# Kernel optimization log

Hardware: AMD Instinct MI355X
Metric: run time of the kernel (lower is better)

Reference implementation:

```python
import jax, jax.numpy as jnp
import numpy as np

B, T, V, E, H, DE = 64, 52, 10000, 512, 512, 2048


def _lstm_cell(x, h, c, w_ih, w_hh, b_ih, b_hh):
    # torch.nn.LSTMCell gate order: i, f, g, o
    gates = x @ w_ih.T + h @ w_hh.T + b_ih + b_hh
    i, f, g, o = jnp.split(gates, 4, axis=-1)
    c2 = jax.nn.sigmoid(f) * c + jax.nn.sigmoid(i) * jnp.tanh(g)
    h2 = jax.nn.sigmoid(o) * jnp.tanh(c2)
    return h2, c2


def _run_dir(emb_seq, img, lens, p1, p2, fc_w, fc_b):
    # emb_seq: [B, Td, E]; img: [B, H]; lens: [B] sorted descending.
    # The torch loop slices h[:batch_size_t]; since lens is sorted descending,
    # that is equivalent to masking updates where t >= (len-1). Rows that fall
    # out of the active prefix are never read again, and their predictions stay 0.
    Bd, Td = emb_seq.shape[0], emb_seq.shape[1]
    Hd = img.shape[1]
    mask = jnp.arange(Td)[None, :] < (lens - 1)[:, None]  # [B, Td]
    z = jnp.zeros((Bd, Hd), emb_seq.dtype)

    def step(carry, xs):
        h, c, h1, c1 = carry
        x, m = xs
        m2 = m[:, None]
        hn, cn = _lstm_cell(x, h, c, *p1)
        h1n, c1n = _lstm_cell(jnp.concatenate([hn, img], axis=1), h1, c1, *p2)
        carry = (jnp.where(m2, hn, h), jnp.where(m2, cn, c),
                 jnp.where(m2, h1n, h1), jnp.where(m2, c1n, c1))
        preds = jnp.where(m2, h1n @ fc_w.T + fc_b, 0.0)  # [B, V]
        return carry, preds

    _, preds = jax.lax.scan(step, (z, z, z, z), (emb_seq.transpose(1, 0, 2), mask.T))
    return preds.transpose(1, 0, 2)  # [B, Td, V]


def setup_inputs():
    key = jax.random.key(0)
    ks = iter(jax.random.split(key, 48))

    def u(shape, a=-0.1, b=0.1):
        return jax.random.uniform(next(ks), shape, minval=a, maxval=b, dtype=jnp.float32)

    inp = {}
    inp['encoder_out'] = jax.random.normal(next(ks), (B, DE), dtype=jnp.float32)
    inp['encoded_captions'] = jax.random.randint(next(ks), (B, T), 0, V)
    cl = jax.random.randint(next(ks), (B, 1), 2, T + 1)
    inp['caption_lengths'] = cl.at[0, 0].set(T)  # ensure max decode length = T-1
    # embeddings (uniform -0.1..0.1 per init_weights)
    inp['emb_w'] = u((V, E))
    inp['emb_r_w'] = u((V, E))
    # LSTM cells: torch default init uniform(-1/sqrt(H), 1/sqrt(H))
    kH = 1.0 / np.sqrt(H)
    for name, din in [('1', E), ('2', 2 * H), ('r1', E), ('r2', 2 * H)]:
        inp['w_ih' + name] = u((4 * H, din), -kH, kH)
        inp['w_hh' + name] = u((4 * H, H), -kH, kH)
        inp['b_ih' + name] = u((4 * H,), -kH, kH)
        inp['b_hh' + name] = u((4 * H,), -kH, kH)
    kD = 1.0 / np.sqrt(DE)
    inp['img_f_w'] = u((H, DE), -kD, kD)
    inp['img_f_b'] = u((H,), -kD, kD)
    inp['img_b_w'] = u((H, DE), -kD, kD)
    inp['img_b_b'] = u((H,), -kD, kD)
    inp['fc_w'] = u((V, H))
    inp['fc_b'] = jnp.zeros((V,), jnp.float32)
    inp['fcr_w'] = u((V, H))
    inp['fcr_b'] = jnp.zeros((V,), jnp.float32)
    return inp


def reference(encoder_out, encoded_captions, caption_lengths, emb_w, emb_r_w,
              w_ih1, w_hh1, b_ih1, b_hh1, w_ih2, w_hh2, b_ih2, b_hh2,
              w_ihr1, w_hhr1, b_ihr1, b_hhr1, w_ihr2, w_hhr2, b_ihr2, b_hhr2,
              img_f_w, img_f_b, img_b_w, img_b_b, fc_w, fc_b, fcr_w, fcr_b):
    lens = caption_lengths[:, 0]
    order = jnp.argsort(-lens)  # descending, stable (jax argsort is stable)
    lens = lens[order]
    enc = encoder_out[order]
    caps = encoded_captions[order]
    Tc = caps.shape[1]
    # per-row reversal of the first len tokens; rest zero (matches torch loop)
    j = jnp.arange(Tc)[None, :]
    valid = j < lens[:, None]
    rev_idx = jnp.where(valid, lens[:, None] - 1 - j, 0)
    caps_rev = jnp.where(valid, jnp.take_along_axis(caps, rev_idx, axis=1), 0)
    emb = emb_w[caps]          # [B, T, E]
    emb_r = emb_r_w[caps_rev]  # [B, T, E]
    img_f = enc @ img_f_w.T + img_f_b
    img_r = enc @ img_b_w.T + img_b_b
    Td = Tc - 1  # max(decode_lengths); setup guarantees max(lens) == T
    preds = _run_dir(emb[:, :Td], img_f, lens,
                     (w_ih1, w_hh1, b_ih1, b_hh1), (w_ih2, w_hh2, b_ih2, b_hh2), fc_w, fc_b)
    preds_r = _run_dir(emb_r[:, :Td], img_r, lens,
                       (w_ihr1, w_hhr1, b_ihr1, b_hhr1), (w_ihr2, w_hhr2, b_ihr2, b_hhr2), fcr_w, fcr_b)
    return preds, preds_r, caps, caps_rev, lens - 1, order
```

## Files before the change

kernel.cpp:

```cpp
#include <hip/hip_runtime.h>
#include <stdint.h>

#define B64   64
#define T52   52
#define TD    51
#define V10K  10000
#define MP    3328
#define MR    3264
#define NPFC  10112

typedef float  f32x4  __attribute__((ext_vector_type(4)));
typedef __bf16 bf16x8 __attribute__((ext_vector_type(8)));
typedef unsigned int u32x4 __attribute__((ext_vector_type(4)));
typedef unsigned short ushort_t;

__device__ inline unsigned short f2bf(float f) {
  unsigned u = __builtin_bit_cast(unsigned, f);
  u += 0x7fffu + ((u >> 16) & 1u);
  return (unsigned short)(u >> 16);
}
__device__ inline unsigned pack2(float a, float b) {
  return (unsigned)f2bf(a) | ((unsigned)f2bf(b) << 16);
}
__device__ inline float sigm(float x) { return 1.f / (1.f + expf(-x)); }

__device__ inline void store2_sc(ushort_t* p, unsigned v) {
  asm volatile("global_store_short %0, %1, off sc1" :: "v"(p), "v"(v) : "memory");
}
__device__ inline void loadA16(const ushort_t* a, u32x4 (&h)[16]) {
  asm volatile(
    "global_load_dwordx4 %0,  %16, off sc1\n\t"
    "global_load_dwordx4 %1,  %16, off offset:64 sc1\n\t"
    "global_load_dwordx4 %2,  %16, off offset:128 sc1\n\t"
    "global_load_dwordx4 %3,  %16, off offset:192 sc1\n\t"
    "global_load_dwordx4 %4,  %16, off offset:256 sc1\n\t"
    "global_load_dwordx4 %5,  %16, off offset:320 sc1\n\t"
    "global_load_dwordx4 %6,  %16, off offset:384 sc1\n\t"
    "global_load_dwordx4 %7,  %16, off offset:448 sc1\n\t"
    "global_load_dwordx4 %8,  %16, off offset:512 sc1\n\t"
    "global_load_dwordx4 %9,  %16, off offset:576 sc1\n\t"
    "global_load_dwordx4 %10, %16, off offset:640 sc1\n\t"
    "global_load_dwordx4 %11, %16, off offset:704 sc1\n\t"
    "global_load_dwordx4 %12, %16, off offset:768 sc1\n\t"
    "global_load_dwordx4 %13, %16, off offset:832 sc1\n\t"
    "global_load_dwordx4 %14, %16, off offset:896 sc1\n\t"
    "global_load_dwordx4 %15, %16, off offset:960 sc1\n\t"
    "s_waitcnt vmcnt(0)"
    : "=&v"(h[0]),"=&v"(h[1]),"=&v"(h[2]),"=&v"(h[3]),
      "=&v"(h[4]),"=&v"(h[5]),"=&v"(h[6]),"=&v"(h[7]),
      "=&v"(h[8]),"=&v"(h[9]),"=&v"(h[10]),"=&v"(h[11]),
      "=&v"(h[12]),"=&v"(h[13]),"=&v"(h[14]),"=&v"(h[15])
    : "v"(a) : "memory");
}
__device__ inline void loadA32(const ushort_t* a, const ushort_t* b,
                               u32x4 (&ha)[16], u32x4 (&hb)[16]) {
  asm volatile(
    "global_load_dwordx4 %0,  %32, off sc1\n\t"
    "global_load_dwordx4 %1,  %32, off offset:64 sc1\n\t"
    "global_load_dwordx4 %2,  %32, off offset:128 sc1\n\t"
    "global_load_dwordx4 %3,  %32, off offset:192 sc1\n\t"
    "global_load_dwordx4 %4,  %32, off offset:256 sc1\n\t"
    "global_load_dwordx4 %5,  %32, off offset:320 sc1\n\t"
    "global_load_dwordx4 %6,  %32, off offset:384 sc1\n\t"
    "global_load_dwordx4 %7,  %32, off offset:448 sc1\n\t"
    "global_load_dwordx4 %8,  %32, off offset:512 sc1\n\t"
    "global_load_dwordx4 %9,  %32, off offset:576 sc1\n\t"
    "global_load_dwordx4 %10, %32, off offset:640 sc1\n\t"
    "global_load_dwordx4 %11, %32, off offset:704 sc1\n\t"
    "global_load_dwordx4 %12, %32, off offset:768 sc1\n\t"
    "global_load_dwordx4 %13, %32, off offset:832 sc1\n\t"
    "global_load_dwordx4 %14, %32, off offset:896 sc1\n\t"
    "global_load_dwordx4 %15, %32, off offset:960 sc1\n\t"
    "global_load_dwordx4 %16, %33, off sc1\n\t"
    "global_load_dwordx4 %17, %33, off offset:64 sc1\n\t"
    "global_load_dwordx4 %18, %33, off offset:128 sc1\n\t"
    "global_load_dwordx4 %19, %33, off offset:192 sc1\n\t"
    "global_load_dwordx4 %20, %33, off offset:256 sc1\n\t"
    "global_load_dwordx4 %21, %33, off offset:320 sc1\n\t"
    "global_load_dwordx4 %22, %33, off offset:384 sc1\n\t"
    "global_load_dwordx4 %23, %33, off offset:448 sc1\n\t"
    "global_load_dwordx4 %24, %33, off offset:512 sc1\n\t"
    "global_load_dwordx4 %25, %33, off offset:576 sc1\n\t"
    "global_load_dwordx4 %26, %33, off offset:640 sc1\n\t"
    "global_load_dwordx4 %27, %33, off offset:704 sc1\n\t"
    "global_load_dwordx4 %28, %33, off offset:768 sc1\n\t"
    "global_load_dwordx4 %29, %33, off offset:832 sc1\n\t"
    "global_load_dwordx4 %30, %33, off offset:896 sc1\n\t"
    "global_load_dwordx4 %31, %33, off offset:960 sc1\n\t"
    "s_waitcnt vmcnt(0)"
    : "=&v"(ha[0]),"=&v"(ha[1]),"=&v"(ha[2]),"=&v"(ha[3]),
      "=&v"(ha[4]),"=&v"(ha[5]),"=&v"(ha[6]),"=&v"(ha[7]),
      "=&v"(ha[8]),"=&v"(ha[9]),"=&v"(ha[10]),"=&v"(ha[11]),
      "=&v"(ha[12]),"=&v"(ha[13]),"=&v"(ha[14]),"=&v"(ha[15]),
      "=&v"(hb[0]),"=&v"(hb[1]),"=&v"(hb[2]),"=&v"(hb[3]),
      "=&v"(hb[4]),"=&v"(hb[5]),"=&v"(hb[6]),"=&v"(hb[7]),
      "=&v"(hb[8]),"=&v"(hb[9]),"=&v"(hb[10]),"=&v"(hb[11]),
      "=&v"(hb[12]),"=&v"(hb[13]),"=&v"(hb[14]),"=&v"(hb[15])
    : "v"(a), "v"(b) : "memory");
}

__global__ void k_prep(const int* __restrict__ cl, const int* __restrict__ caps,
                       float* __restrict__ out_caps, float* __restrict__ out_capr,
                       float* __restrict__ out_lm1, float* __restrict__ out_ord,
                       int* __restrict__ order_i, int* __restrict__ lensm1_i,
                       int* __restrict__ nvtab, int* __restrict__ capsS,
                       int* __restrict__ capsRev, int* __restrict__ cumtab,
                       int* __restrict__ rowmap)
{
  __shared__ int L[64], O[64], Ls_s[64], Cum[65];
  __shared__ int C_s[64][T52];
  int i = threadIdx.x;
  L[i] = cl[i];
  __syncthreads();
  if (i == 0) {
    for (int a = 0; a < 64; ++a) O[a] = a;
    for (int a = 1; a < 64; ++a) {
      int key = O[a], kl = L[key], b = a - 1;
      while (b >= 0 && L[O[b]] < kl) { O[b + 1] = O[b]; --b; }
      O[b + 1] = key;
    }
  }
  __syncthreads();
  int src = O[i];
  int Ls  = L[src];
  Ls_s[i] = Ls;
  order_i[i]  = src;
  lensm1_i[i] = Ls - 1;
  out_lm1[i]  = (float)(Ls - 1);
  out_ord[i]  = (float)src;
  for (int t = 0; t < T52; ++t) {
    int c = caps[src * T52 + t];
    C_s[i][t] = c;
    capsS[i * T52 + t]    = c;
    out_caps[i * T52 + t] = (float)c;
  }
  __syncthreads();
  for (int j = 0; j < T52; ++j) {
    int rv = (j < Ls) ? C_s[i][Ls - 1 - j] : 0;
    capsRev[i * T52 + j]  = rv;
    out_capr[i * T52 + j] = (float)rv;
  }
  if (i == 0) {
    int s = 0;
    for (int b = 0; b < 64; ++b) { Cum[b] = s; s += Ls_s[b] - 1; }
    Cum[64] = s;
  }
  __syncthreads();
  cumtab[i] = Cum[i];
  if (i == 0) cumtab[64] = Cum[64];
  for (int t = 0; t < Ls - 1; ++t) rowmap[Cum[i] + t] = i * TD + t;
  {
    int Mc = Cum[64];
    int invBase = Mc + i * TD - Cum[i];
    for (int t = Ls - 1; t < TD; ++t)
      rowmap[invBase + (t - (Ls - 1))] = i * TD + t;
  }
  if (i < TD) {
    int nv = 0;
    for (int r = 0; r < 64; ++r) nv += (Ls_s[r] - 1 > i) ? 1 : 0;
    nvtab[i] = nv;
  }
}

__global__ void k_convert(const float* __restrict__ w_ih1, const float* __restrict__ w_ihr1,
                          const float* __restrict__ fc_w, const float* __restrict__ fcr_w,
                          const float* __restrict__ b_ih1, const float* __restrict__ b_hh1,
                          const float* __restrict__ b_ihr1, const float* __restrict__ b_hhr1,
                          const float* __restrict__ w_hh1, const float* __restrict__ w_hhr1,
                          const float* __restrict__ w_ih2, const float* __restrict__ w_ihr2,
                          const float* __restrict__ w_hh2, const float* __restrict__ w_hhr2,
                          const float* __restrict__ img_f_w, const float* __restrict__ img_b_w,
                          const float* __restrict__ b_ih2, const float* __restrict__ b_hh2,
                          const float* __restrict__ b_ihr2, const float* __restrict__ b_hhr2,
                          const float* __restrict__ enc, const int* __restrict__ order_i,
                          const float* __restrict__ emb_w, const float* __restrict__ emb_r_w,
                          const int* __restrict__ capsS, const int* __restrict__ capsRev,
                          const int* __restrict__ rowmap, const int* __restrict__ cumtab,
                          ushort_t* __restrict__ wih1bf, ushort_t* __restrict__ fcwbf,
                          ushort_t* __restrict__ whh1bf, ushort_t* __restrict__ wih2Lbf,
                          ushort_t* __restrict__ whh2bf, ushort_t* __restrict__ wih2Ibf,
                          ushort_t* __restrict__ imgwbf, ushort_t* __restrict__ encbf,
                          ushort_t* __restrict__ embA,
                          float* __restrict__ biasg1, float* __restrict__ biasg2)
{
  long long gid = (long long)blockIdx.x * blockDim.x + threadIdx.x;
  const long long C1 = 2048LL * 512 / 8;
  const long long CF = (long long)NPFC * 512 / 8;
  const long long CPD = (long long)MP * 512 / 8;
  const long long bs  = 2 * C1 + 2 * CF;
  const long long bs2 = bs + 6 * C1;
  const long long bs3 = bs2 + 2 * C1;
  const long long bs4 = bs3 + 2 * C1;
  const long long bs5 = bs4 + 32768;
  const long long bs6 = bs5 + 2 * CPD;
  if (gid < 2 * C1) {
    int dir = gid >= C1; long long cid = gid - (long long)dir * C1;
    const float* s = (dir ? w_ihr1 : w_ih1) + cid * 8;
    ushort_t* d = wih1bf + (long long)dir * 2048 * 512 + cid * 8;
    uint4 v;
    v.x = pack2(s[0], s[1]); v.y = pack2(s[2], s[3]);
    v.z = pack2(s[4], s[5]); v.w = pack2(s[6], s[7]);
    *(uint4*)d = v;
  } else if (gid < bs) {
    long long g2 = gid - 2 * C1; int dir = g2 >= CF;
    long long cid = g2 - (long long)dir * CF;
    long long row = cid >> 6; int k8 = (int)(cid & 63) * 8;
    ushort_t* d = fcwbf + (long long)dir * NPFC * 512 + row * 512 + k8;
    uint4 v;
    if (row < V10K) {
      const float* s = (dir ? fcr_w : fc_w) + row * 512 + k8;
      v.x = pack2(s[0], s[1]); v.y = pack2(s[2], s[3]);
      v.z = pack2(s[4], s[5]); v.w = pack2(s[6], s[7]);
    } else { v.x = v.y = v.z = v.w = 0u; }
    *(uint4*)d = v;
  } else if (gid < bs2) {
    long long e = gid - bs;
    int arr = (int)(e / (2 * C1));
    long long d2 = e - (long long)arr * 2 * C1;
    int dir = d2 >= C1;
    long long cid = d2 - (long long)dir * C1;
    long long row = cid >> 6; int k8 = (int)(cid & 63) * 8;
    const float* s;
    ushort_t* d;
    if (arr == 0)      { s = (dir ? w_hhr1 : w_hh1) + row * 512  + k8; d = whh1bf; }
    else if (arr == 1) { s = (dir ? w_ihr2 : w_ih2) + row * 1024 + k8; d = wih2Lbf; }
    else               { s = (dir ? w_hhr2 : w_hh2) + row * 512  + k8; d = whh2bf; }
    d += (long long)dir * 2048 * 512 + cid * 8;
    uint4 v;
    v.x = pack2(s[0], s[1]); v.y = pack2(s[2], s[3]);
    v.z = pack2(s[4], s[5]); v.w = pack2(s[6], s[7]);
    *(uint4*)d = v;
  } else if (gid < bs3) {
    long long e = gid - bs2; int dir = e >= C1;
    long long cid = e - (long long)dir * C1;
    long long row = cid >> 6; int k8 = (int)(cid & 63) * 8;
    const float* s = (dir ? w_ihr2 : w_ih2) + row * 1024 + 512 + k8;
    ushort_t* d = wih2Ibf + (long long)dir * 2048 * 512 + cid * 8;
    uint4 v;
    v.x = pack2(s[0], s[1]); v.y = pack2(s[2], s[3]);
    v.z = pack2(s[4], s[5]); v.w = pack2(s[6], s[7]);
    *(uint4*)d = v;
  } else if (gid < bs4) {
    long long e = gid - bs3; int dir = e >= C1;
    long long cid = e - (long long)dir * C1;
    long long row = cid >> 8; int c8 = (int)(cid & 255) * 8;
    const float* s = (dir ? img_b_w : img_f_w) + row * 2048 + c8;
    ushort_t* d = imgwbf + (long long)dir * 512 * 2048 + cid * 8;
    uint4 v;
    v.x = pack2(s[0], s[1]); v.y = pack2(s[2], s[3]);
    v.z = pack2(s[4], s[5]); v.w = pack2(s[6], s[7]);
    *(uint4*)d = v;
  } else if (gid < bs5) {
    long long cid = gid - bs4;
    int m = (int)(cid >> 8); int c8 = (int)(cid & 255) * 8;
    const float* s = enc + (long long)order_i[m & 63] * 2048 + c8;
    ushort_t* d = encbf + cid * 8;
    uint4 v;
    v.x = pack2(s[0], s[1]); v.y = pack2(s[2], s[3]);
    v.z = pack2(s[4], s[5]); v.w = pack2(s[6], s[7]);
    *(uint4*)d = v;
  } else if (gid < bs6) {
    long long e = gid - bs5;
    int dir = e >= CPD; long long cid = e - (long long)dir * CPD;
    int c = (int)(cid >> 6); int k8 = (int)(cid & 63) * 8;
    ushort_t* d = embA + (long long)dir * MP * 512 + (long long)c * 512 + k8;
    uint4 v;
    if (c < cumtab[64]) {
      int m = rowmap[c];
      int b = m / TD, t = m - b * TD;
      int row = dir ? capsRev[b * T52 + t] : capsS[b * T52 + t];
      const float* s = (dir ? emb_r_w : emb_w) + (long long)row * 512 + k8;
      v.x = pack2(s[0], s[1]); v.y = pack2(s[2], s[3]);
      v.z = pack2(s[4], s[5]); v.w = pack2(s[6], s[7]);
    } else { v.x = v.y = v.z = v.w = 0u; }
    *(uint4*)d = v;
  } else {
    long long g3 = gid - bs6;
    if (g3 < 4096) {
      int dir = g3 >= 2048; int j = (int)(g3 & 2047);
      biasg1[dir * 2048 + j] = dir ? (b_ihr1[j] + b_hhr1[j]) : (b_ih1[j] + b_hh1[j]);
    } else if (g3 < 8192) {
      long long g4 = g3 - 4096;
      int dir = g4 >= 2048; int j = (int)(g4 & 2047);
      biasg2[dir * 2048 + j] = dir ? (b_ihr2[j] + b_hhr2[j]) : (b_ih2[j] + b_hh2[j]);
    }
  }
}

template<int MODE>
__global__ __launch_bounds__(256)
void k_gemm(const ushort_t* __restrict__ A0, long long As,
            const ushort_t* __restrict__ B0, long long Bs,
            const float* __restrict__ bias0, const float* __restrict__ bias1,
            void* __restrict__ out0, long long Os,
            int Nreal, int K, const int* __restrict__ mlim)
{
  long long tm = (long long)blockIdx.x * 128;
  if (mlim && tm >= mlim[64]) return;
  __shared__ ushort_t Ab[128 * 32];
  __shared__ ushort_t Bb[128 * 32];
  int dirz = blockIdx.z;
  const ushort_t* A = A0 + dirz * As;
  const ushort_t* Bm = B0 + dirz * Bs;
  const float* bias = dirz ? bias1 : bias0;
  int tid = threadIdx.x;
  int lane = tid & 63, wid = tid >> 6;
  int wr = wid >> 1, wc = wid & 1;
  long long tn = (long long)blockIdx.y * 128;
  f32x4 acc[4][4] = {};
  int c0 = tid, c1 = tid + 256;
  const ushort_t* Ag0 = A + (tm + (c0 >> 2)) * K + (c0 & 3) * 8;
  const ushort_t* Ag1 = A + (tm + (c1 >> 2)) * K + (c1 & 3) * 8;
  const ushort_t* Bg0 = Bm + (tn + (c0 >> 2)) * K + (c0 & 3) * 8;
  const ushort_t* Bg1 = Bm + (tn + (c1 >> 2)) * K + (c1 & 3) * 8;
  int KK = K >> 5;
  for (int kk = 0; kk < KK; ++kk) {
    uint4 va0 = *(const uint4*)(Ag0 + kk * 32);
    uint4 va1 = *(const uint4*)(Ag1 + kk * 32);
    uint4 vb0 = *(const uint4*)(Bg0 + kk * 32);
    uint4 vb1 = *(const uint4*)(Bg1 + kk * 32);
    __syncthreads();
    *(uint4*)&Ab[c0 * 8] = va0;
    *(uint4*)&Ab[c1 * 8] = va1;
    *(uint4*)&Bb[c0 * 8] = vb0;
    *(uint4*)&Bb[c1 * 8] = vb1;
    __syncthreads();
    int koff = (lane >> 4) * 8;
    bf16x8 av[4], bv[4];
    #pragma unroll
    for (int mi = 0; mi < 4; ++mi)
      av[mi] = *(const bf16x8*)&Ab[(wr * 64 + mi * 16 + (lane & 15)) * 32 + koff];
    #pragma unroll
    for (int ni = 0; ni < 4; ++ni)
      bv[ni] = *(const bf16x8*)&Bb[(wc * 64 + ni * 16 + (lane & 15)) * 32 + koff];
    #pragma unroll
    for (int mi = 0; mi < 4; ++mi)
      #pragma unroll
      for (int ni = 0; ni < 4; ++ni)
        acc[mi][ni] = __builtin_amdgcn_mfma_f32_16x16x32_bf16(av[mi], bv[ni], acc[mi][ni], 0, 0, 0);
  }
  #pragma unroll
  for (int mi = 0; mi < 4; ++mi) {
    #pragma unroll
    for (int rr = 0; rr < 4; ++rr) {
      long long m = tm + wr * 64 + mi * 16 + ((lane >> 4) * 4) + rr;
      if (MODE == 0) {
        float* orow = (float*)out0 + dirz * Os + m * (long long)Nreal;
        #pragma unroll
        for (int ni = 0; ni < 4; ++ni) {
          int n = (int)tn + wc * 64 + ni * 16 + (lane & 15);
          orow[n] = acc[mi][ni][rr] + bias[n];
        }
      } else if (MODE == 2) {
        float bm = bias[m];
        float* orow = (float*)out0 + dirz * Os + m * (long long)Nreal;
        #pragma unroll
        for (int ni = 0; ni < 4; ++ni) {
          int n = (int)tn + wc * 64 + ni * 16 + (lane & 15);
          if (n < Nreal) orow[n] = acc[mi][ni][rr] + bm;
        }
      } else {
        ushort_t* orow = (ushort_t*)out0 + dirz * Os + m * (long long)Nreal;
        #pragma unroll
        for (int ni = 0; ni < 4; ++ni) {
          int n = (int)tn + wc * 64 + ni * 16 + (lane & 15);
          orow[n] = f2bf(acc[mi][ni][rr] + bias[n]);
        }
      }
    }
  }
}

__global__ __launch_bounds__(256)
void k_fc(const ushort_t* __restrict__ A0, const ushort_t* __restrict__ B0,
          const float* __restrict__ bias0, const float* __restrict__ bias1,
          float* __restrict__ out0, const int* __restrict__ rowmap,
          const int* __restrict__ cumtab)
{
  const long long PRED = (long long)MR * V10K;
  int Mc = cumtab[64];
  int bid = blockIdx.x;
  int xcd = bid & 7, slot = bid >> 3;
  int q = slot / 26, mi = slot % 26;
  int G = xcd + 8 * q;
  if (G >= 158) return;
  int dirz = G & 1, ni = G >> 1;
  long long tm = (long long)mi * 128;
  long long tn = (long long)ni * 128;
  float* out = out0 + (long long)dirz * PRED;
  int tid = threadIdx.x;
  if (tm >= Mc) {
    int row = tid >> 1, hf = tid & 1;
    long long c = tm + row;
    if (c < MR) {
      int m = rowmap[c];
      float* orow = out + (long long)m * V10K;
      float4 z = {0.f, 0.f, 0.f, 0.f};
      int col0 = (int)tn + hf * 64;
      #pragma unroll
      for (int qq = 0; qq < 16; ++qq) {
        int col = col0 + qq * 4;
        if (col < V10K) *(float4*)(orow + col) = z;
      }
    }
    return;
  }
  __shared__ ushort_t Ab[128 * 32];
  __shared__ ushort_t Bb[128 * 32];
  const ushort_t* A = A0 + (long long)dirz * MP * 512;
  const ushort_t* Bm = B0 + (long long)dirz * NPFC * 512;
  const float* bias = dirz ? bias1 : bias0;
  int lane = tid & 63, wid = tid >> 6;
  int wr = wid >> 1, wc = wid & 1;
  f32x4 acc[4][4] = {};
  int c0 = tid, c1 = tid + 256;
  const ushort_t* Ag0 = A + (tm + (c0 >> 2)) * 512 + (c0 & 3) * 8;
  const ushort_t* Ag1 = A + (tm + (c1 >> 2)) * 512 + (c1 & 3) * 8;
  const ushort_t* Bg0 = Bm + (tn + (c0 >> 2)) * 512 + (c0 & 3) * 8;
  const ushort_t* Bg1 = Bm + (tn + (c1 >> 2)) * 512 + (c1 & 3) * 8;
  for (int kk = 0; kk < 16; ++kk) {
    uint4 va0 = *(const uint4*)(Ag0 + kk * 32);
    uint4 va1 = *(const uint4*)(Ag1 + kk * 32);
    uint4 vb0 = *(const uint4*)(Bg0 + kk * 32);
    uint4 vb1 = *(const uint4*)(Bg1 + kk * 32);
    __syncthreads();
    *(uint4*)&Ab[c0 * 8] = va0;
    *(uint4*)&Ab[c1 * 8] = va1;
    *(uint4*)&Bb[c0 * 8] = vb0;
    *(uint4*)&Bb[c1 * 8] = vb1;
    __syncthreads();
    int koff = (lane >> 4) * 8;
    bf16x8 av[4], bv[4];
    #pragma unroll
    for (int mi2 = 0; mi2 < 4; ++mi2)
      av[mi2] = *(const bf16x8*)&Ab[(wr * 64 + mi2 * 16 + (lane & 15)) * 32 + koff];
    #pragma unroll
    for (int ni2 = 0; ni2 < 4; ++ni2)
      bv[ni2] = *(const bf16x8*)&Bb[(wc * 64 + ni2 * 16 + (lane & 15)) * 32 + koff];
    #pragma unroll
    for (int mi2 = 0; mi2 < 4; ++mi2)
      #pragma unroll
      for (int ni2 = 0; ni2 < 4; ++ni2)
        acc[mi2][ni2] = __builtin_amdgcn_mfma_f32_16x16x32_bf16(av[mi2], bv[ni2], acc[mi2][ni2], 0, 0, 0);
  }
  #pragma unroll
  for (int mi2 = 0; mi2 < 4; ++mi2) {
    #pragma unroll
    for (int rr = 0; rr < 4; ++rr) {
      long long c = tm + wr * 64 + mi2 * 16 + ((lane >> 4) * 4) + rr;
      if (c < MR) {
        int m = rowmap[c];
        bool val = (c < Mc);
        float* orow = out + (long long)m * V10K;
        #pragma unroll
        for (int ni2 = 0; ni2 < 4; ++ni2) {
          int n = (int)tn + wc * 64 + ni2 * 16 + (lane & 15);
          if (n < V10K) orow[n] = val ? (acc[mi2][ni2][rr] + bias[n]) : 0.f;
        }
      }
    }
  }
}

__global__ __launch_bounds__(128, 1)
void k_rec(const ushort_t* __restrict__ whh1bf, const ushort_t* __restrict__ wih2Lbf,
           const ushort_t* __restrict__ whh2bf, const float* __restrict__ xg1,
           const float* __restrict__ xg2imgT,
           ushort_t* __restrict__ h1hist,
           ushort_t* __restrict__ h2buf,
           ushort_t* __restrict__ h2allbf,
           const int* __restrict__ nvtab, const int* __restrict__ cumtab,
           int* __restrict__ slots)
{
  const int bid = blockIdx.x;
  const bool isL2 = bid >= 128;
  const int idx = isL2 ? bid - 128 : bid;
  const int dir = idx >> 6, sub = idx & 63, half = sub >> 5, ht = sub & 31;
  const int tid = threadIdx.x;
  const int lane = tid & 63, mt = tid >> 6;
  const int l15 = lane & 15, l4 = lane >> 4;
  const int jl = ht * 16 + l15;
  const int rbase = half * 32 + mt * 16;
  const int r0 = rbase + l4 * 4;

  __shared__ ushort_t Wl[32768];
  __shared__ ushort_t Wi[32768];
  __shared__ int nv_s[64];
  __shared__ int cum_s[64];

  {
    const ushort_t* src = (isL2 ? whh2bf : whh1bf) + (long long)dir * 2048 * 512;
    #pragma unroll
    for (int i = 0; i < 32; ++i) {
      int c = tid + i * 128;
      int nl = c >> 6;
      int kb = (c & 63) * 16;
      int row = (nl >> 4) * 512 + ht * 16 + (nl & 15);
      u32x4 v = *(const u32x4*)(src + (long long)row * 512 + (long long)(c & 63) * 8);
      *(u32x4*)((char*)Wl + nl * 1024 + (kb ^ ((nl & 7) << 4))) = v;
    }
    if (isL2) {
      const ushort_t* src2 = wih2Lbf + (long long)dir * 2048 * 512;
      #pragma unroll
      for (int i = 0; i < 32; ++i) {
        int c = tid + i * 128;
        int nl = c >> 6;
        int kb = (c & 63) * 16;
        int row = (nl >> 4) * 512 + ht * 16 + (nl & 15);
        u32x4 v = *(const u32x4*)(src2 + (long long)row * 512 + (long long)(c & 63) * 8);
        *(u32x4*)((char*)Wi + nl * 1024 + (kb ^ ((nl & 7) << 4))) = v;
      }
    }
    if (tid < TD) nv_s[tid] = nvtab[tid];
    if (tid < 64) cum_s[tid] = cumtab[tid];
  }
  __syncthreads();

  int* aS = slots + (dir * 2 + half) * 32;
  int* bS = slots + 128 + (dir * 2 + half) * 32;

  if (!isL2) {
    f32x4 creg = {0.f, 0.f, 0.f, 0.f};
    for (int t = 0; t < TD; ++t) {
      bool act = (rbase < nv_s[t]);
      float xs[4][4];
      if (act) {
        const float* xb = xg1 + (long long)dir * MP * 2048;
        #pragma unroll
        for (int rr = 0; rr < 4; ++rr) {
          const float* xr = xb + (long long)(cum_s[r0 + rr] + t) * 2048;
          #pragma unroll
          for (int g = 0; g < 4; ++g)
            xs[g][rr] = xr[g * 512 + jl];
        }
      }
      if (t > 0) {
        if (mt == 0) {
          for (;;) {
            int v = __hip_atomic_load(&aS[lane & 31], __ATOMIC_RELAXED, __HIP_MEMORY_SCOPE_AGENT);
            if (__all(v >= t)) break;
          }
        }
        __syncthreads();
      }
      if (act) {
        const ushort_t* hsrc = h1hist + ((long long)t * 2 + dir) * (64 * 512);
        u32x4 hv[16];
        loadA16(hsrc + (long long)(rbase + l15) * 512 + l4 * 8, hv);
        f32x4 acc[4] = {};
        #pragma unroll
        for (int kk = 0; kk < 16; ++kk) {
          bf16x8 av = __builtin_bit_cast(bf16x8, hv[kk]);
          int kb = kk * 64 + l4 * 16;
          #pragma unroll
          for (int g = 0; g < 4; ++g) {
            bf16x8 bv = *(const bf16x8*)((const char*)Wl + (g * 16 + l15) * 1024 + (kb ^ ((l15 & 7) << 4)));
            acc[g] = __builtin_amdgcn_mfma_f32_16x16x32_bf16(av, bv, acc[g], 0, 0, 0);
          }
        }
        ushort_t* hdst = h1hist + ((long long)(t + 1) * 2 + dir) * (64 * 512);
        f32x4 cn;
        #pragma unroll
        for (int rr = 0; rr < 4; ++rr) {
          float gi = acc[0][rr] + xs[0][rr];
          float gf = acc[1][rr] + xs[1][rr];
          float gg = acc[2][rr] + xs[2][rr];
          float go = acc[3][rr] + xs[3][rr];
          float c = sigm(gf) * creg[rr] + sigm(gi) * tanhf(gg);
          float h = sigm(go) * tanhf(c);
          cn[rr] = c;
          store2_sc(hdst + (long long)(r0 + rr) * 512 + jl, (unsigned)f2bf(h));
        }
        creg = cn;
      }
      __syncthreads();
      if (tid == 0)
        __hip_atomic_store(&aS[ht], t + 1, __ATOMIC_RELAXED, __HIP_MEMORY_SCOPE_AGENT);
    }
  } else {
    f32x4 xv2[4];
    {
      const float* xg = xg2imgT + (long long)dir * (2048 * 64);
      #pragma unroll
      for (int g = 0; g < 4; ++g)
        xv2[g] = *(const f32x4*)(xg + (long long)(g * 512 + jl) * 64 + r0);
    }
    f32x4 creg = {0.f, 0.f, 0.f, 0.f};
    for (int t = 0; t < TD; ++t) {
      if (mt == 0) {
        for (;;) {
          int va = __hip_atomic_load(&aS[lane & 31], __ATOMIC_RELAXED, __HIP_MEMORY_SCOPE_AGENT);
          int vb = __hip_atomic_load(&bS[lane & 31], __ATOMIC_RELAXED, __HIP_MEMORY_SCOPE_AGENT);
          if (__all((va >= t + 1) & (vb >= t))) break;
        }
      }
      __syncthreads();
      int nv = nv_s[t];
      if (rbase < nv) {
        const ushort_t* h1s = h1hist + ((long long)(t + 1) * 2 + dir) * (64 * 512);
        const ushort_t* h2s = h2buf + ((long long)((t + 1) & 1) * 2 + dir) * (64 * 512);
        u32x4 ha[16], hb[16];
        loadA32(h1s + (long long)(rbase + l15) * 512 + l4 * 8,
                h2s + (long long)(rbase + l15) * 512 + l4 * 8, ha, hb);
        f32x4 acc[4] = {};
        #pragma unroll
        for (int kk = 0; kk < 16; ++kk) {
          bf16x8 av = __builtin_bit_cast(bf16x8, ha[kk]);
          int kb = kk * 64 + l4 * 16;
          #pragma unroll
          for (int g = 0; g < 4; ++g) {
            bf16x8 bv = *(const bf16x8*)((const char*)Wi + (g * 16 + l15) * 1024 + (kb ^ ((l15 & 7) << 4)));
            acc[g] = __builtin_amdgcn_mfma_f32_16x16x32_bf16(av, bv, acc[g], 0, 0, 0);
          }
        }
        #pragma unroll
        for (int kk = 0; kk < 16; ++kk) {
          bf16x8 av = __builtin_bit_cast(bf16x8, hb[kk]);
          int kb = kk * 64 + l4 * 16;
          #pragma unroll
          for (int g = 0; g < 4; ++g) {
            bf16x8 bv = *(const bf16x8*)((const char*)Wl + (g * 16 + l15) * 1024 + (kb ^ ((l15 & 7) << 4)));
            acc[g] = __builtin_amdgcn_mfma_f32_16x16x32_bf16(av, bv, acc[g], 0, 0, 0);
          }
        }
        ushort_t* h2n = h2buf + ((long long)(t & 1) * 2 + dir) * (64 * 512);
        ushort_t* h2a = h2allbf + (long long)dir * MP * 512;
        f32x4 cn;
        #pragma unroll
        for (int rr = 0; rr < 4; ++rr) {
          float gi = acc[0][rr] + xv2[0][rr];
          float gf = acc[1][rr] + xv2[1][rr];
          float gg = acc[2][rr] + xv2[2][rr];
          float go = acc[3][rr] + xv2[3][rr];
          float c = sigm(gf) * creg[rr] + sigm(gi) * tanhf(gg);
          float h = sigm(go) * tanhf(c);
          cn[rr] = c;
          ushort_t hbb = f2bf(h);
          store2_sc(h2n + (long long)(r0 + rr) * 512 + jl, (unsigned)hbb);
          if (r0 + rr < nv)
            h2a[((long long)(cum_s[r0 + rr] + t)) * 512 + jl] = hbb;
        }
        creg = cn;
      }
      __syncthreads();
      if (tid == 0)
        __hip_atomic_store(&bS[ht], t + 1, __ATOMIC_RELAXED, __HIP_MEMORY_SCOPE_AGENT);
    }
  }
}

extern "C" void kernel_launch(void* const* d_in, const int* in_sizes, int n_in,
                              void* d_out, int out_size, void* d_ws, size_t ws_size,
                              hipStream_t stream)
{
  const float* enc     = (const float*)d_in[0];
  const int*   caps    = (const int*)d_in[1];
  const int*   cl      = (const int*)d_in[2];
  const float* emb_w   = (const float*)d_in[3];
  const float* emb_r_w = (const float*)d_in[4];
  const float* w_ih1   = (const float*)d_in[5];
  const float* w_hh1   = (const float*)d_in[6];
  const float* b_ih1   = (const float*)d_in[7];
  const float* b_hh1   = (const float*)d_in[8];
  const float* w_ih2   = (const float*)d_in[9];
  const float* w_hh2   = (const float*)d_in[10];
  const float* b_ih2   = (const float*)d_in[11];
  const float* b_hh2   = (const float*)d_in[12];
  const float* w_ihr1  = (const float*)d_in[13];
  const float* w_hhr1  = (const float*)d_in[14];
  const float* b_ihr1  = (const float*)d_in[15];
  const float* b_hhr1  = (const float*)d_in[16];
  const float* w_ihr2  = (const float*)d_in[17];
  const float* w_hhr2  = (const float*)d_in[18];
  const float* b_ihr2  = (const float*)d_in[19];
  const float* b_hhr2  = (const float*)d_in[20];
  const float* img_f_w = (const float*)d_in[21];
  const float* img_f_b = (const float*)d_in[22];
  const float* img_b_w = (const float*)d_in[23];
  const float* img_b_b = (const float*)d_in[24];
  const float* fc_w    = (const float*)d_in[25];
  const float* fc_b    = (const float*)d_in[26];
  const float* fcr_w   = (const float*)d_in[27];
  const float* fcr_b   = (const float*)d_in[28];

  float* outF = (float*)d_out;
  const long long PRED = (long long)MR * V10K;
  float* o_caps = outF + 2 * PRED;
  float* o_capr = o_caps + B64 * T52;
  float* o_lm1  = o_capr + B64 * T52;
  float* o_ord  = o_lm1 + B64;
  float*    xg1       = outF;
  ushort_t* whh1bf    = (ushort_t*)(outF + 27500000);
  ushort_t* wih2Lbf   = (ushort_t*)(outF + 28600000);
  ushort_t* whh2bf    = (ushort_t*)(outF + 29700000);
  ushort_t* h1hist    = (ushort_t*)(outF + 31000000);
  ushort_t* wih2Ibf   = (ushort_t*)(outF + 34600000);
  ushort_t* imgwbf    = (ushort_t*)(outF + 35700000);
  ushort_t* encbf     = (ushort_t*)(outF + 36800000);
  ushort_t* imgbf     = (ushort_t*)(outF + 37000000);

  char* w = (char*)d_ws;
  auto alloc = [&](size_t bytes) -> char* {
    char* p = w; w += (bytes + 255) & ~(size_t)255; return p;
  };
  int*      order_i  = (int*)alloc(64 * 4);
  int*      lensm1_i = (int*)alloc(64 * 4);
  int*      nvtab    = (int*)alloc(64 * 4);
  int*      cumtab   = (int*)alloc(65 * 4);
  int*      rowmap   = (int*)alloc(MR * 4);
  int*      capsS    = (int*)alloc(B64 * T52 * 4);
  int*      capsRev  = (int*)alloc(B64 * T52 * 4);
  float*    biasg1   = (float*)alloc(2 * 2048 * 4);
  float*    biasg2   = (float*)alloc(2 * 2048 * 4);
  float*    xg2imgT  = (float*)alloc((size_t)2 * 2048 * 64 * 4);
  char*     stateBase = alloc(262144 + 1024);
  ushort_t* h2buf = (ushort_t*)stateBase;
  int*      slotp = (int*)(stateBase + 262144);
  ushort_t* embA    = (ushort_t*)alloc((size_t)2 * MP * 512 * 2);
  ushort_t* wih1bf  = (ushort_t*)alloc((size_t)2 * 2048 * 512 * 2);
  ushort_t* fcwbf   = (ushort_t*)alloc((size_t)2 * NPFC * 512 * 2);
  ushort_t* h2allbf = (ushort_t*)alloc((size_t)2 * MP * 512 * 2);

  hipMemsetAsync(stateBase, 0, 262144 + 1024, stream);
  hipMemsetAsync(h1hist, 0, 131072, stream);

  k_prep<<<1, 64, 0, stream>>>(cl, caps, o_caps, o_capr, o_lm1, o_ord,
                               order_i, lensm1_i, nvtab, capsS, capsRev,
                               cumtab, rowmap);
  k_convert<<<13024, 256, 0, stream>>>(w_ih1, w_ihr1, fc_w, fcr_w,
                                       b_ih1, b_hh1, b_ihr1, b_hhr1,
                                       w_hh1, w_hhr1, w_ih2, w_ihr2, w_hh2, w_hhr2,
                                       img_f_w, img_b_w, b_ih2, b_hh2, b_ihr2, b_hhr2,
                                       enc, order_i, emb_w, emb_r_w,
                                       capsS, capsRev, rowmap, cumtab,
                                       wih1bf, fcwbf, whh1bf, wih2Lbf, whh2bf,
                                       wih2Ibf, imgwbf, encbf, embA, biasg1, biasg2);
  k_gemm<3><<<dim3(1, 4, 2), 256, 0, stream>>>(encbf, 0LL,
                                               imgwbf, 512LL * 2048,
                                               img_f_b, img_b_b,
                                               imgbf, 128LL * 512,
                                               512, 2048, nullptr);
  k_gemm<2><<<dim3(16, 1, 2), 256, 0, stream>>>(wih2Ibf, 2048LL * 512,
                                                imgbf, 128LL * 512,
                                                biasg2, biasg2 + 2048,
                                                xg2imgT, 2048LL * 64,
                                                64, 512, nullptr);
  k_gemm<0><<<dim3(26, 16, 2), 256, 0, stream>>>(embA, (long long)MP * 512,
                                                 wih1bf, 2048LL * 512,
                                                 biasg1, biasg1 + 2048,
                                                 xg1, (long long)MP * 2048,
                                                 2048, 512, cumtab);
  k_rec<<<256, 128, 0, stream>>>(whh1bf, wih2Lbf, whh2bf, xg1, xg2imgT,
                                 h1hist, h2buf, h2allbf, nvtab, cumtab, slotp);
  k_fc<<<4160, 256, 0, stream>>>(h2allbf, fcwbf, fc_b, fcr_b,
                                 outF, rowmap, cumtab);
}
```

Baseline: 693.9 us.

## Fold state memsets into convert kernel, defer h2 history stores, simplify fc grid

The two hipMemsetAsync calls that zero the recurrent state and h1 history are replaced by extra threads in the convert kernel, which removes two launches. In the recurrent kernel, the scatter of h2 into the history buffer now happens after the step-completion flag is published, taking it off the critical path between steps. The fc kernel drops its XCD-aware block swizzle in favour of a plain 3D grid, which changes L2 locality across chiplets and may lose weight reuse.

```diff
diff --git a/kernel.cpp b/kernel.cpp
--- a/kernel.cpp
+++ b/kernel.cpp
@@ -181,7 +181,8 @@
                           ushort_t* __restrict__ whh2bf, ushort_t* __restrict__ wih2Ibf,
                           ushort_t* __restrict__ imgwbf, ushort_t* __restrict__ encbf,
                           ushort_t* __restrict__ embA,
-                          float* __restrict__ biasg1, float* __restrict__ biasg2)
+                          float* __restrict__ biasg1, float* __restrict__ biasg2,
+                          char* __restrict__ stateBase, char* __restrict__ h1hist0)
 {
   long long gid = (long long)blockIdx.x * blockDim.x + threadIdx.x;
   const long long C1 = 2048LL * 512 / 8;
@@ -193,6 +194,7 @@
   const long long bs4 = bs3 + 2 * C1;
   const long long bs5 = bs4 + 32768;
   const long long bs6 = bs5 + 2 * CPD;
+  const long long bs7 = bs6 + 8192;
   if (gid < 2 * C1) {
     int dir = gid >= C1; long long cid = gid - (long long)dir * C1;
     const float* s = (dir ? w_ihr1 : w_ih1) + cid * 8;
@@ -274,15 +276,23 @@
       v.z = pack2(s[4], s[5]); v.w = pack2(s[6], s[7]);
     } else { v.x = v.y = v.z = v.w = 0u; }
     *(uint4*)d = v;
-  } else {
+  } else if (gid < bs7) {
     long long g3 = gid - bs6;
     if (g3 < 4096) {
       int dir = g3 >= 2048; int j = (int)(g3 & 2047);
       biasg1[dir * 2048 + j] = dir ? (b_ihr1[j] + b_hhr1[j]) : (b_ih1[j] + b_hh1[j]);
-    } else if (g3 < 8192) {
+    } else {
       long long g4 = g3 - 4096;
       int dir = g4 >= 2048; int j = (int)(g4 & 2047);
       biasg2[dir * 2048 + j] = dir ? (b_ihr2[j] + b_hhr2[j]) : (b_ih2[j] + b_hh2[j]);
+    }
+  } else {
+    long long z = gid - bs7;
+    uint4 zero = {0u, 0u, 0u, 0u};
+    if (z < 16448) {
+      ((uint4*)stateBase)[z] = zero;
+    } else if (z < 16448 + 8192) {
+      ((uint4*)h1hist0)[z - 16448] = zero;
     }
   }
 }
@@ -379,14 +389,9 @@
 {
   const long long PRED = (long long)MR * V10K;
   int Mc = cumtab[64];
-  int bid = blockIdx.x;
-  int xcd = bid & 7, slot = bid >> 3;
-  int q = slot / 26, mi = slot % 26;
-  int G = xcd + 8 * q;
-  if (G >= 158) return;
-  int dirz = G & 1, ni = G >> 1;
-  long long tm = (long long)mi * 128;
-  long long tn = (long long)ni * 128;
+  long long tm = (long long)blockIdx.x * 128;
+  int dirz = blockIdx.z;
+  long long tn = (long long)blockIdx.y * 128;
   float* out = out0 + (long long)dirz * PRED;
   int tid = threadIdx.x;
   if (tm >= Mc) {
@@ -596,7 +601,9 @@
       }
       __syncthreads();
       int nv = nv_s[t];
-      if (rbase < nv) {
+      bool act = (rbase < nv);
+      ushort_t hb4[4];
+      if (act) {
         const ushort_t* h1s = h1hist + ((long long)(t + 1) * 2 + dir) * (64 * 512);
         const ushort_t* h2s = h2buf + ((long long)((t + 1) & 1) * 2 + dir) * (64 * 512);
         u32x4 ha[16], hb[16];
@@ -624,7 +631,6 @@
           }
         }
         ushort_t* h2n = h2buf + ((long long)(t & 1) * 2 + dir) * (64 * 512);
-        ushort_t* h2a = h2allbf + (long long)dir * MP * 512;
         f32x4 cn;
         #pragma unroll
         for (int rr = 0; rr < 4; ++rr) {
@@ -636,15 +642,21 @@
           float h = sigm(go) * tanhf(c);
           cn[rr] = c;
           ushort_t hbb = f2bf(h);
+          hb4[rr] = hbb;
           store2_sc(h2n + (long long)(r0 + rr) * 512 + jl, (unsigned)hbb);
-          if (r0 + rr < nv)
-            h2a[((long long)(cum_s[r0 + rr] + t)) * 512 + jl] = hbb;
         }
         creg = cn;
       }
       __syncthreads();
       if (tid == 0)
         __hip_atomic_store(&bS[ht], t + 1, __ATOMIC_RELAXED, __HIP_MEMORY_SCOPE_AGENT);
+      if (act) {
+        ushort_t* h2a = h2allbf + (long long)dir * MP * 512;
+        #pragma unroll
+        for (int rr = 0; rr < 4; ++rr)
+          if (r0 + rr < nv)
+            h2a[((long long)(cum_s[r0 + rr] + t)) * 512 + jl] = hb4[rr];
+      }
     }
   }
 }
@@ -721,20 +733,18 @@
   ushort_t* fcwbf   = (ushort_t*)alloc((size_t)2 * NPFC * 512 * 2);
   ushort_t* h2allbf = (ushort_t*)alloc((size_t)2 * MP * 512 * 2);
 
-  hipMemsetAsync(stateBase, 0, 262144 + 1024, stream);
-  hipMemsetAsync(h1hist, 0, 131072, stream);
-
   k_prep<<<1, 64, 0, stream>>>(cl, caps, o_caps, o_capr, o_lm1, o_ord,
                                order_i, lensm1_i, nvtab, capsS, capsRev,
                                cumtab, rowmap);
-  k_convert<<<13024, 256, 0, stream>>>(w_ih1, w_ihr1, fc_w, fcr_w,
+  k_convert<<<13121, 256, 0, stream>>>(w_ih1, w_ihr1, fc_w, fcr_w,
                                        b_ih1, b_hh1, b_ihr1, b_hhr1,
                                        w_hh1, w_hhr1, w_ih2, w_ihr2, w_hh2, w_hhr2,
                                        img_f_w, img_b_w, b_ih2, b_hh2, b_ihr2, b_hhr2,
                                        enc, order_i, emb_w, emb_r_w,
                                        capsS, capsRev, rowmap, cumtab,
                                        wih1bf, fcwbf, whh1bf, wih2Lbf, whh2bf,
-                                       wih2Ibf, imgwbf, encbf, embA, biasg1, biasg2);
+                                       wih2Ibf, imgwbf, encbf, embA, biasg1, biasg2,
+                                       stateBase, (char*)h1hist);
   k_gemm<3><<<dim3(1, 4, 2), 256, 0, stream>>>(encbf, 0LL,
                                                imgwbf, 512LL * 2048,
                                                img_f_b, img_b_b,
@@ -752,6 +762,6 @@
                                                  2048, 512, cumtab);
   k_rec<<<256, 128, 0, stream>>>(whh1bf, wih2Lbf, whh2bf, xg1, xg2imgT,
                                  h1hist, h2buf, h2allbf, nvtab, cumtab, slotp);
-  k_fc<<<4160, 256, 0, stream>>>(h2allbf, fcwbf, fc_b, fcr_b,
-                                 outF, rowmap, cumtab);
-}
+  k_fc<<<dim3(26, 79, 2), 256, 0, stream>>>(h2allbf, fcwbf, fc_b, fcr_b,
+                                            outF, rowmap, cumtab);
+}
```

New measurement: 680.8 us. Within noise of the previous version (-1.9%).
